# Performance work log

Hardware: AMD Instinct MI355X
Metric: run time of the kernel (lower is better)

Reference implementation:

```python
import jax, jax.numpy as jnp
import numpy as np

B, N, C = 64, 512, 1280


def setup_inputs() -> dict:
    key = jax.random.key(0)
    ks = jax.random.split(key, 10)
    scale = 0.02
    x = jax.random.normal(ks[0], (B, N, C), dtype=jnp.float32)
    Mask = jax.random.randint(ks[1], (B, N, N), 0, 2, dtype=jnp.int32)
    Wq = jax.random.normal(ks[2], (C, C), dtype=jnp.float32) * scale
    bq = jnp.zeros((C,), dtype=jnp.float32)
    Wk = jax.random.normal(ks[3], (C, C), dtype=jnp.float32) * scale
    bk = jnp.zeros((C,), dtype=jnp.float32)
    Wv = jax.random.normal(ks[4], (C, C), dtype=jnp.float32) * scale
    bv = jnp.zeros((C,), dtype=jnp.float32)
    Wr = jax.random.normal(ks[5], (C, C), dtype=jnp.float32) * scale
    br = jnp.zeros((C,), dtype=jnp.float32)
    return {"x": x, "Mask": Mask, "Wq": Wq, "bq": bq, "Wk": Wk, "bk": bk,
            "Wv": Wv, "bv": bv, "Wr": Wr, "br": br}


def reference(x, Mask, Wq, bq, Wk, bk, Wv, bv, Wr, br):
    # q, k, v: [B, N, C]
    q = x @ Wq + bq
    k = x @ Wk + bk
    v = x @ Wv + bv
    # scores[b, n, m] = q[b, n] . k[b, m]  -> [B, N, N]
    scores = jnp.einsum('bnc,bmc->bnm', q, k)
    # masked_fill BEFORE the scale divide, as in the original module
    scores = jnp.where(Mask == 0, jnp.float32(-1e20), scores)
    attn = jax.nn.softmax(scores / jnp.sqrt(jnp.float32(C)), axis=-1)
    # original: (V^T @ attn).permute -> out[b, n, c] = sum_m v[b, m, c] * attn[b, m, n]
    att_feat = jnp.einsum('bmc,bmn->bnc', v, attn)
    return att_feat @ Wr + br
```

## Files before the change

### kernel.cpp

```cpp
#include <hip/hip_runtime.h>
#include <hip/hip_bf16.h>

#define DI __device__ __forceinline__

typedef __attribute__((ext_vector_type(8))) short short8;
typedef __attribute__((ext_vector_type(4))) float f32x4;

DI unsigned short f2bf(float f) {
    union { float f; unsigned int u; } v; v.f = f;
    unsigned int r = v.u + 0x7FFFu + ((v.u >> 16) & 1u);
    return (unsigned short)(r >> 16);
}
DI float bf2f(unsigned short h) {
    union { unsigned int u; float f; } v; v.u = ((unsigned int)h) << 16;
    return v.f;
}

#define GLD16(g, l) __builtin_amdgcn_global_load_lds( \
    (const __attribute__((address_space(1))) void*)(g), \
    (__attribute__((address_space(3))) void*)(l), 16, 0, 0)

template<int EPI, int QKV>
__global__ __launch_bounds__(512, 2) void gemm256(
    const unsigned short* __restrict__ A, const unsigned short* __restrict__ Bt,
    void* __restrict__ Cout, const float* __restrict__ bias,
    const float* __restrict__ bias1, const float* __restrict__ bias2,
    const int* __restrict__ mask, int K, int lda, int ldb, int ldc,
    long sA, long sB, long sC, long sM, float scale)
{
    __shared__ unsigned short lds[65536];

    const unsigned gx = gridDim.x, gy = gridDim.y;
    unsigned lin = blockIdx.x + gx * (blockIdx.y + gy * blockIdx.z);
    const unsigned nwg = gx * gy * gridDim.z;
    lin = (lin & 7u) * (nwg >> 3) + (lin >> 3);
    int tn = lin % gx;
    const int tm = (lin / gx) % gy;
    const int z = lin / (gx * gy);

    if (QKV) {
        const int g = tn / 5; tn -= g * 5;
        Bt += (size_t)g * sB;
        Cout = (void*)((unsigned short*)Cout + (size_t)g * sC);
        if (g == 1) bias = bias1; else if (g == 2) bias = bias2;
    }

    const unsigned short* Ab = A + (long)z * sA + (size_t)(tm * 256) * lda;
    const unsigned short* Bb = Bt + (QKV ? 0 : (long)z * sB) + (size_t)(tn * 256) * ldb;

    const int tid = threadIdx.x, wave = tid >> 6, l = tid & 63;
    const int wr = wave >> 2, wc = wave & 3;

    const int srow = wave * 32 + (l >> 2);
    const int schunk = ((l & 3) ^ ((l >> 3) & 3)) * 8;
    const unsigned short* agS = Ab + (size_t)srow * lda + schunk;
    const unsigned short* bgS = Bb + (size_t)srow * ldb + schunk;
    unsigned short* ldsA0 = &lds[wave * 1024];
    unsigned short* ldsB0 = &lds[8192 + wave * 1024];

    const int rl = l & 15;
    const int cl8 = ((l >> 4) ^ ((l >> 1) & 3)) * 8;
    const int aoff = (wr * 128 + rl) * 32 + cl8;
    const int boff = 8192 + (wc * 64 + rl) * 32 + cl8;

#define REGOFF(buf, h) (((buf) * 2 + (h)) * 16384)
#define SA(t, h, buf) { const unsigned short* g_ = agS + (size_t)((t) * 64 + (h) * 32); \
    GLD16(g_, ldsA0 + REGOFF(buf, h)); \
    GLD16(g_ + (size_t)16 * lda, ldsA0 + REGOFF(buf, h) + 512); }
#define SB(t, h, buf) { const unsigned short* g_ = bgS + (size_t)((t) * 64 + (h) * 32); \
    GLD16(g_, ldsB0 + REGOFF(buf, h)); \
    GLD16(g_ + (size_t)16 * ldb, ldsB0 + REGOFF(buf, h) + 512); }

    f32x4 acc[8][4] = {};
    short8 bfr[4];

#define PHASE(mg, h, buf, RDB, STG, VMW) { \
    short8 af[4]; \
    if (RDB) { \
        _Pragma("unroll") for (int n = 0; n < 4; ++n) \
            bfr[n] = *(const short8*)&lds[REGOFF(buf, h) + boff + n * 512]; \
    } \
    _Pragma("unroll") for (int i = 0; i < 4; ++i) \
        af[i] = *(const short8*)&lds[REGOFF(buf, h) + aoff + ((mg) * 4 + i) * 512]; \
    STG; \
    __builtin_amdgcn_s_barrier(); \
    asm volatile("s_waitcnt lgkmcnt(0)" ::: "memory"); \
    __builtin_amdgcn_sched_barrier(0); \
    __builtin_amdgcn_s_setprio(1); \
    _Pragma("unroll") for (int i = 0; i < 4; ++i) \
        _Pragma("unroll") for (int n = 0; n < 4; ++n) \
            acc[(mg) * 4 + i][n] = __builtin_amdgcn_mfma_f32_16x16x32_bf16( \
                af[i], bfr[n], acc[(mg) * 4 + i][n], 0, 0, 0); \
    __builtin_amdgcn_s_setprio(0); \
    asm volatile("s_waitcnt " VMW ::: "memory"); \
    __builtin_amdgcn_s_barrier(); \
  }

    SA(0, 0, 0); SB(0, 0, 0); SA(0, 1, 0); SB(0, 1, 0); SA(1, 0, 1); SB(1, 0, 1);
    asm volatile("s_waitcnt vmcnt(8)" ::: "memory");
    __builtin_amdgcn_s_barrier();

    const int NI = K >> 7;
    for (int j = 0; j < NI - 1; ++j) {
        const int t = 2 * j;
        PHASE(0, 0, 0, 1, SA(t + 1, 1, 1), "vmcnt(8)")
        PHASE(1, 0, 0, 0, SB(t + 1, 1, 1), "vmcnt(8)")
        PHASE(0, 1, 0, 1, SA(t + 2, 0, 0), "vmcnt(8)")
        PHASE(1, 1, 0, 0, SB(t + 2, 0, 0), "vmcnt(8)")
        PHASE(0, 0, 1, 1, SA(t + 2, 1, 0), "vmcnt(8)")
        PHASE(1, 0, 1, 0, SB(t + 2, 1, 0), "vmcnt(8)")
        PHASE(0, 1, 1, 1, SA(t + 3, 0, 1), "vmcnt(8)")
        PHASE(1, 1, 1, 0, SB(t + 3, 0, 1), "vmcnt(8)")
    }
    {
        const int t = 2 * (NI - 1);
        PHASE(0, 0, 0, 1, SA(t + 1, 1, 1), "vmcnt(8)")
        PHASE(1, 0, 0, 0, SB(t + 1, 1, 1), "vmcnt(8)")
        PHASE(0, 1, 0, 1, ((void)0),       "vmcnt(8)")
        PHASE(1, 1, 0, 0, ((void)0),       "vmcnt(4)")
        PHASE(0, 0, 1, 1, ((void)0),       "vmcnt(4)")
        PHASE(1, 0, 1, 0, ((void)0),       "vmcnt(0)")
        PHASE(0, 1, 1, 1, ((void)0),       "vmcnt(0)")
        PHASE(1, 1, 1, 0, ((void)0),       "vmcnt(0)")
    }
#undef PHASE
#undef SA
#undef SB
#undef REGOFF

    const long cb = QKV ? 0 : (long)z * sC;
    const int row0 = tm * 256 + wr * 128 + (l >> 4) * 4;
    const int col0 = tn * 256 + wc * 64 + rl;
    #pragma unroll
    for (int mi = 0; mi < 8; ++mi) {
        #pragma unroll
        for (int n = 0; n < 4; ++n) {
            #pragma unroll
            for (int r = 0; r < 4; ++r) {
                const int row = row0 + mi * 16 + r;
                const int col = col0 + n * 16;
                float v = acc[mi][n][r];
                if (EPI == 0 || EPI == 3) v += bias[col];
                if (EPI == 1) {
                    v *= scale;
                    if (mask[(long)z * sM + (long)row * ldc + col] == 0)
                        v = -1e20f * scale;
                }
                if (EPI == 3)
                    ((float*)Cout)[cb + (long)row * ldc + col] = v;
                else
                    ((unsigned short*)Cout)[cb + (long)row * ldc + col] = f2bf(v);
            }
        }
    }
}

__global__ void transpose_w(const float* __restrict__ Wq, const float* __restrict__ Wk,
                            const float* __restrict__ Wv, const float* __restrict__ Wr,
                            unsigned short* __restrict__ Wt)
{
    const float* W = blockIdx.z == 0 ? Wq : blockIdx.z == 1 ? Wk : blockIdx.z == 2 ? Wv : Wr;
    unsigned short* dst = Wt + (size_t)blockIdx.z * 1280 * 1280;
    __shared__ float T[64][65];
    const int j0 = blockIdx.x * 64, k0 = blockIdx.y * 64;
    const int tid = threadIdx.x;
    for (int it = 0; it < 16; ++it) {
        int idx = it * 256 + tid;
        int r = idx >> 6, c = idx & 63;
        T[r][c] = W[(size_t)(k0 + r) * 1280 + j0 + c];
    }
    __syncthreads();
    for (int it = 0; it < 16; ++it) {
        int idx = it * 256 + tid;
        int r = idx >> 6, c = idx & 63;
        dst[(size_t)(j0 + r) * 1280 + k0 + c] = f2bf(T[c][r]);
    }
}

__global__ void cast_x(const float* __restrict__ x, unsigned short* __restrict__ xb, long n)
{
    long i = ((long)blockIdx.x * 256 + threadIdx.x) * 8;
    if (i + 8 > n) return;
    const float4* p = (const float4*)(x + i);
    float4 a = p[0], b = p[1];
    unsigned short o[8] = { f2bf(a.x), f2bf(a.y), f2bf(a.z), f2bf(a.w),
                            f2bf(b.x), f2bf(b.y), f2bf(b.z), f2bf(b.w) };
    *(short8*)(xb + i) = *(short8*)o;
}

#define SMS 514
__global__ void softmax_t(const unsigned short* __restrict__ S, unsigned short* __restrict__ Pt)
{
    __shared__ unsigned short T[64 * SMS];
    __shared__ float rmax[64], rinv[64];
    const int b = blockIdx.y, mb = blockIdx.x * 64;
    const int tid = threadIdx.x, lane = tid & 63, wave = tid >> 6;
    const unsigned short* src = S + ((size_t)b * 512 + mb) * 512;

    for (int rr = 0; rr < 16; ++rr) {
        int r = rr * 4 + wave;
        const unsigned int* s = (const unsigned int*)(src + (size_t)r * 512);
        unsigned int* t = (unsigned int*)&T[r * SMS];
        #pragma unroll
        for (int j = 0; j < 4; ++j) t[lane + j * 64] = s[lane + j * 64];
    }
    __syncthreads();

    {
        int r = tid >> 2, q = tid & 3;
        const unsigned short* row = &T[r * SMS + q * 128];
        float mx = -3.0e38f;
        for (int i = 0; i < 128; ++i) mx = fmaxf(mx, bf2f(row[i]));
        mx = fmaxf(mx, __shfl_xor(mx, 1));
        mx = fmaxf(mx, __shfl_xor(mx, 2));
        float s = 0.f;
        for (int i = 0; i < 128; ++i) s += expf(bf2f(row[i]) - mx);
        s += __shfl_xor(s, 1);
        s += __shfl_xor(s, 2);
        if (q == 0) { rmax[r] = mx; rinv[r] = 1.0f / s; }
    }
    __syncthreads();

    {
        int m = tid & 63, nq = tid >> 6;
        float mxm = rmax[m], rim = rinv[m];
        unsigned short* dst = Pt + (size_t)b * 512 * 512 + mb + m;
        for (int it = 0; it < 128; ++it) {
            int n = it * 4 + nq;
            float v = expf(bf2f(T[m * SMS + n]) - mxm) * rim;
            dst[(size_t)n * 512] = f2bf(v);
        }
    }
}

__global__ void transpose_v(const unsigned short* __restrict__ V, unsigned short* __restrict__ Vt)
{
    __shared__ unsigned short T[64][65];
    const int b = blockIdx.z;
    const int c0 = blockIdx.x * 64, m0 = blockIdx.y * 64;
    const int tid = threadIdx.x;
    const unsigned short* src = V + ((size_t)b * 512 + m0) * 1280 + c0;
    for (int it = 0; it < 16; ++it) {
        int idx = it * 256 + tid;
        int r = idx >> 6, c = idx & 63;
        T[r][c] = src[(size_t)r * 1280 + c];
    }
    __syncthreads();
    unsigned short* dst = Vt + ((size_t)b * 1280 + c0) * 512 + m0;
    for (int it = 0; it < 16; ++it) {
        int idx = it * 256 + tid;
        int r = idx >> 6, c = idx & 63;
        dst[(size_t)r * 512 + c] = T[c][r];
    }
}

extern "C" void kernel_launch(void* const* d_in, const int* in_sizes, int n_in,
                              void* d_out, int out_size, void* d_ws, size_t ws_size,
                              hipStream_t stream)
{
    const float* x   = (const float*)d_in[0];
    const int*  Mask = (const int*)d_in[1];
    const float* Wq  = (const float*)d_in[2];
    const float* bq  = (const float*)d_in[3];
    const float* Wk  = (const float*)d_in[4];
    const float* bk  = (const float*)d_in[5];
    const float* Wv  = (const float*)d_in[6];
    const float* bv  = (const float*)d_in[7];
    const float* Wr  = (const float*)d_in[8];
    const float* br  = (const float*)d_in[9];

    constexpr int N = 512, C = 1280;
    constexpr long MN = 32768;

    char* ws = (char*)d_ws;
    unsigned short* xb = (unsigned short*)ws;
    unsigned short* Wt = (unsigned short*)(ws + 83886080);
    unsigned short* Q  = (unsigned short*)(ws + 83886080 + 13107200);
    unsigned short* Km = Q + 41943040;
    unsigned short* V  = Km + 41943040;
    unsigned short* Sp = V + 41943040;
    unsigned short* Pt = Sp + 16777216;
    unsigned short* Vt = Q;
    unsigned short* att = xb;

    const float scale = 0.02795084971874737f;

    transpose_w<<<dim3(20, 20, 4), 256, 0, stream>>>(Wq, Wk, Wv, Wr, Wt);
    cast_x<<<dim3(20480), 256, 0, stream>>>(x, xb, MN * C);

    gemm256<0, 1><<<dim3(15, 128, 1), 512, 0, stream>>>(xb, Wt, (void*)Q, bq, bk, bv,
        nullptr, C, C, C, C, 0, 1638400L, 41943040L, 0, 0.f);

    gemm256<1, 0><<<dim3(2, 2, 64), 512, 0, stream>>>(Q, Km, (void*)Sp, nullptr, nullptr, nullptr,
        Mask, C, C, C, N, (long)N * C, (long)N * C, (long)N * N, (long)N * N, scale);

    softmax_t<<<dim3(8, 64), 256, 0, stream>>>(Sp, Pt);

    transpose_v<<<dim3(20, 8, 64), 256, 0, stream>>>(V, Vt);

    gemm256<2, 0><<<dim3(5, 2, 64), 512, 0, stream>>>(Pt, Vt, (void*)att, nullptr, nullptr, nullptr,
        nullptr, N, N, N, C, (long)N * N, (long)C * N, (long)N * C, 0, 0.f);

    gemm256<3, 0><<<dim3(5, 128, 1), 512, 0, stream>>>(att, Wt + 3 * 1638400, d_out, br, nullptr, nullptr,
        nullptr, C, C, C, C, 0, 0, 0, 0, 0.f);
}
```

Before: 722.5 us.

## Double-buffer LDS fragment registers to overlap reads with MFMA in GEMM

Restructures the GEMM main loop so the A/B fragments for the next phase are read from LDS into a second register set while the MFMAs for the current phase run, with one barrier per phase placed after the compute. The vmcnt waits are retuned to match the new staging order, and a final compute-only phase is added. Epilogue stores become nontemporal to reduce cache pollution. Doubling the fragment registers raises register pressure under launch_bounds(512,2), which could cause spills.

```diff
diff --git a/kernel.cpp b/kernel.cpp
--- a/kernel.cpp
+++ b/kernel.cpp
@@ -72,58 +72,72 @@
     GLD16(g_ + (size_t)16 * ldb, ldsB0 + REGOFF(buf, h) + 512); }
 
     f32x4 acc[8][4] = {};
-    short8 bfr[4];
-
-#define PHASE(mg, h, buf, RDB, STG, VMW) { \
-    short8 af[4]; \
-    if (RDB) { \
+    short8 af0[4], af1[4], bf0[4], bf1[4];
+
+#define PHASE(MGC, CUR, NXT, MGN, HN, BUFN, STG, VMW) { \
+    if (MGN == 0) { \
         _Pragma("unroll") for (int n = 0; n < 4; ++n) \
-            bfr[n] = *(const short8*)&lds[REGOFF(buf, h) + boff + n * 512]; \
+            bf##NXT[n] = *(const short8*)&lds[REGOFF(BUFN, HN) + boff + n * 512]; \
+    } else { \
+        _Pragma("unroll") for (int n = 0; n < 4; ++n) bf##NXT[n] = bf##CUR[n]; \
     } \
     _Pragma("unroll") for (int i = 0; i < 4; ++i) \
-        af[i] = *(const short8*)&lds[REGOFF(buf, h) + aoff + ((mg) * 4 + i) * 512]; \
+        af##NXT[i] = *(const short8*)&lds[REGOFF(BUFN, HN) + aoff + ((MGN) * 4 + i) * 512]; \
     STG; \
-    __builtin_amdgcn_s_barrier(); \
-    asm volatile("s_waitcnt lgkmcnt(0)" ::: "memory"); \
     __builtin_amdgcn_sched_barrier(0); \
     __builtin_amdgcn_s_setprio(1); \
     _Pragma("unroll") for (int i = 0; i < 4; ++i) \
         _Pragma("unroll") for (int n = 0; n < 4; ++n) \
-            acc[(mg) * 4 + i][n] = __builtin_amdgcn_mfma_f32_16x16x32_bf16( \
-                af[i], bfr[n], acc[(mg) * 4 + i][n], 0, 0, 0); \
+            acc[(MGC) * 4 + i][n] = __builtin_amdgcn_mfma_f32_16x16x32_bf16( \
+                af##CUR[i], bf##CUR[n], acc[(MGC) * 4 + i][n], 0, 0, 0); \
     __builtin_amdgcn_s_setprio(0); \
     asm volatile("s_waitcnt " VMW ::: "memory"); \
+    asm volatile("s_waitcnt lgkmcnt(0)" ::: "memory"); \
+    __builtin_amdgcn_sched_barrier(0); \
     __builtin_amdgcn_s_barrier(); \
+  }
+#define PHASELAST(MGC, CUR) { \
+    __builtin_amdgcn_s_setprio(1); \
+    _Pragma("unroll") for (int i = 0; i < 4; ++i) \
+        _Pragma("unroll") for (int n = 0; n < 4; ++n) \
+            acc[(MGC) * 4 + i][n] = __builtin_amdgcn_mfma_f32_16x16x32_bf16( \
+                af##CUR[i], bf##CUR[n], acc[(MGC) * 4 + i][n], 0, 0, 0); \
+    __builtin_amdgcn_s_setprio(0); \
   }
 
     SA(0, 0, 0); SB(0, 0, 0); SA(0, 1, 0); SB(0, 1, 0); SA(1, 0, 1); SB(1, 0, 1);
     asm volatile("s_waitcnt vmcnt(8)" ::: "memory");
     __builtin_amdgcn_s_barrier();
+    #pragma unroll
+    for (int n = 0; n < 4; ++n) bf0[n] = *(const short8*)&lds[REGOFF(0, 0) + boff + n * 512];
+    #pragma unroll
+    for (int i = 0; i < 4; ++i) af0[i] = *(const short8*)&lds[REGOFF(0, 0) + aoff + i * 512];
 
     const int NI = K >> 7;
     for (int j = 0; j < NI - 1; ++j) {
         const int t = 2 * j;
-        PHASE(0, 0, 0, 1, SA(t + 1, 1, 1), "vmcnt(8)")
-        PHASE(1, 0, 0, 0, SB(t + 1, 1, 1), "vmcnt(8)")
-        PHASE(0, 1, 0, 1, SA(t + 2, 0, 0), "vmcnt(8)")
-        PHASE(1, 1, 0, 0, SB(t + 2, 0, 0), "vmcnt(8)")
-        PHASE(0, 0, 1, 1, SA(t + 2, 1, 0), "vmcnt(8)")
-        PHASE(1, 0, 1, 0, SB(t + 2, 1, 0), "vmcnt(8)")
-        PHASE(0, 1, 1, 1, SA(t + 3, 0, 1), "vmcnt(8)")
-        PHASE(1, 1, 1, 0, SB(t + 3, 0, 1), "vmcnt(8)")
+        PHASE(0, 0, 1, 1, 0, 0, SA(t + 1, 1, 1), "vmcnt(6)")
+        PHASE(1, 1, 0, 0, 1, 0, SB(t + 1, 1, 1), "vmcnt(6)")
+        PHASE(0, 0, 1, 1, 1, 0, SA(t + 2, 0, 0), "vmcnt(6)")
+        PHASE(1, 1, 0, 0, 0, 1, SB(t + 2, 0, 0), "vmcnt(6)")
+        PHASE(0, 0, 1, 1, 0, 1, SA(t + 2, 1, 0), "vmcnt(6)")
+        PHASE(1, 1, 0, 0, 1, 1, SB(t + 2, 1, 0), "vmcnt(6)")
+        PHASE(0, 0, 1, 1, 1, 1, SA(t + 3, 0, 1), "vmcnt(6)")
+        PHASE(1, 1, 0, 0, 0, 0, SB(t + 3, 0, 1), "vmcnt(6)")
     }
     {
         const int t = 2 * (NI - 1);
-        PHASE(0, 0, 0, 1, SA(t + 1, 1, 1), "vmcnt(8)")
-        PHASE(1, 0, 0, 0, SB(t + 1, 1, 1), "vmcnt(8)")
-        PHASE(0, 1, 0, 1, ((void)0),       "vmcnt(8)")
-        PHASE(1, 1, 0, 0, ((void)0),       "vmcnt(4)")
-        PHASE(0, 0, 1, 1, ((void)0),       "vmcnt(4)")
-        PHASE(1, 0, 1, 0, ((void)0),       "vmcnt(0)")
-        PHASE(0, 1, 1, 1, ((void)0),       "vmcnt(0)")
-        PHASE(1, 1, 1, 0, ((void)0),       "vmcnt(0)")
+        PHASE(0, 0, 1, 1, 0, 0, SA(t + 1, 1, 1), "vmcnt(6)")
+        PHASE(1, 1, 0, 0, 1, 0, SB(t + 1, 1, 1), "vmcnt(6)")
+        PHASE(0, 0, 1, 1, 1, 0, ((void)0),       "vmcnt(4)")
+        PHASE(1, 1, 0, 0, 0, 1, ((void)0),       "vmcnt(2)")
+        PHASE(0, 0, 1, 1, 0, 1, ((void)0),       "vmcnt(0)")
+        PHASE(1, 1, 0, 0, 1, 1, ((void)0),       "vmcnt(0)")
+        PHASE(0, 0, 1, 1, 1, 1, ((void)0),       "vmcnt(0)")
+        PHASELAST(1, 1)
     }
 #undef PHASE
+#undef PHASELAST
 #undef SA
 #undef SB
 #undef REGOFF
@@ -147,9 +161,9 @@
                         v = -1e20f * scale;
                 }
                 if (EPI == 3)
-                    ((float*)Cout)[cb + (long)row * ldc + col] = v;
+                    __builtin_nontemporal_store(v, &((float*)Cout)[cb + (long)row * ldc + col]);
                 else
-                    ((unsigned short*)Cout)[cb + (long)row * ldc + col] = f2bf(v);
+                    __builtin_nontemporal_store(f2bf(v), &((unsigned short*)Cout)[cb + (long)row * ldc + col]);
             }
         }
     }
```

After: 820.2 us. 1.14x slower.

## Merge GEMM phases into four per iteration with split LDS waits

Applied to the files above, without the earlier changes.

Cuts the eight half-tile phases per K iteration to four. Each phase now loads all eight A fragments and the four B fragments, issues both the A and B global-to-LDS stage loads, and runs 32 MFMAs. The barrier before compute is dropped and a partial lgkmcnt(4) wait lets the first 16 MFMAs start while the last A fragment reads are still in flight. This halves the barrier and waitcnt count per tile. In exchange it holds more fragment registers, and removing the pre-compute barrier depends on the remaining barriers and the vmcnt waits being enough to keep the double-buffered LDS safe.

```diff
diff --git a/kernel.cpp b/kernel.cpp
--- a/kernel.cpp
+++ b/kernel.cpp
@@ -72,25 +72,29 @@
     GLD16(g_ + (size_t)16 * ldb, ldsB0 + REGOFF(buf, h) + 512); }
 
     f32x4 acc[8][4] = {};
-    short8 bfr[4];
-
-#define PHASE(mg, h, buf, RDB, STG, VMW) { \
-    short8 af[4]; \
-    if (RDB) { \
-        _Pragma("unroll") for (int n = 0; n < 4; ++n) \
-            bfr[n] = *(const short8*)&lds[REGOFF(buf, h) + boff + n * 512]; \
-    } \
+
+#define PHASE(buf, h, STG, VMW) { \
+    short8 af[8], bfv[4]; \
     _Pragma("unroll") for (int i = 0; i < 4; ++i) \
-        af[i] = *(const short8*)&lds[REGOFF(buf, h) + aoff + ((mg) * 4 + i) * 512]; \
+        af[i] = *(const short8*)&lds[REGOFF(buf, h) + aoff + i * 512]; \
+    _Pragma("unroll") for (int n = 0; n < 4; ++n) \
+        bfv[n] = *(const short8*)&lds[REGOFF(buf, h) + boff + n * 512]; \
+    _Pragma("unroll") for (int i = 4; i < 8; ++i) \
+        af[i] = *(const short8*)&lds[REGOFF(buf, h) + aoff + i * 512]; \
     STG; \
-    __builtin_amdgcn_s_barrier(); \
-    asm volatile("s_waitcnt lgkmcnt(0)" ::: "memory"); \
+    asm volatile("s_waitcnt lgkmcnt(4)" ::: "memory"); \
     __builtin_amdgcn_sched_barrier(0); \
     __builtin_amdgcn_s_setprio(1); \
     _Pragma("unroll") for (int i = 0; i < 4; ++i) \
         _Pragma("unroll") for (int n = 0; n < 4; ++n) \
-            acc[(mg) * 4 + i][n] = __builtin_amdgcn_mfma_f32_16x16x32_bf16( \
-                af[i], bfr[n], acc[(mg) * 4 + i][n], 0, 0, 0); \
+            acc[i][n] = __builtin_amdgcn_mfma_f32_16x16x32_bf16( \
+                af[i], bfv[n], acc[i][n], 0, 0, 0); \
+    asm volatile("s_waitcnt lgkmcnt(0)" ::: "memory"); \
+    __builtin_amdgcn_sched_barrier(0); \
+    _Pragma("unroll") for (int i = 4; i < 8; ++i) \
+        _Pragma("unroll") for (int n = 0; n < 4; ++n) \
+            acc[i][n] = __builtin_amdgcn_mfma_f32_16x16x32_bf16( \
+                af[i], bfv[n], acc[i][n], 0, 0, 0); \
     __builtin_amdgcn_s_setprio(0); \
     asm volatile("s_waitcnt " VMW ::: "memory"); \
     __builtin_amdgcn_s_barrier(); \
@@ -103,25 +107,17 @@
     const int NI = K >> 7;
     for (int j = 0; j < NI - 1; ++j) {
         const int t = 2 * j;
-        PHASE(0, 0, 0, 1, SA(t + 1, 1, 1), "vmcnt(8)")
-        PHASE(1, 0, 0, 0, SB(t + 1, 1, 1), "vmcnt(8)")
-        PHASE(0, 1, 0, 1, SA(t + 2, 0, 0), "vmcnt(8)")
-        PHASE(1, 1, 0, 0, SB(t + 2, 0, 0), "vmcnt(8)")
-        PHASE(0, 0, 1, 1, SA(t + 2, 1, 0), "vmcnt(8)")
-        PHASE(1, 0, 1, 0, SB(t + 2, 1, 0), "vmcnt(8)")
-        PHASE(0, 1, 1, 1, SA(t + 3, 0, 1), "vmcnt(8)")
-        PHASE(1, 1, 1, 0, SB(t + 3, 0, 1), "vmcnt(8)")
+        PHASE(0, 0, SA(t + 1, 1, 1) SB(t + 1, 1, 1), "vmcnt(8)")
+        PHASE(0, 1, SA(t + 2, 0, 0) SB(t + 2, 0, 0), "vmcnt(8)")
+        PHASE(1, 0, SA(t + 2, 1, 0) SB(t + 2, 1, 0), "vmcnt(8)")
+        PHASE(1, 1, SA(t + 3, 0, 1) SB(t + 3, 0, 1), "vmcnt(8)")
     }
     {
         const int t = 2 * (NI - 1);
-        PHASE(0, 0, 0, 1, SA(t + 1, 1, 1), "vmcnt(8)")
-        PHASE(1, 0, 0, 0, SB(t + 1, 1, 1), "vmcnt(8)")
-        PHASE(0, 1, 0, 1, ((void)0),       "vmcnt(8)")
-        PHASE(1, 1, 0, 0, ((void)0),       "vmcnt(4)")
-        PHASE(0, 0, 1, 1, ((void)0),       "vmcnt(4)")
-        PHASE(1, 0, 1, 0, ((void)0),       "vmcnt(0)")
-        PHASE(0, 1, 1, 1, ((void)0),       "vmcnt(0)")
-        PHASE(1, 1, 1, 0, ((void)0),       "vmcnt(0)")
+        PHASE(0, 0, SA(t + 1, 1, 1) SB(t + 1, 1, 1), "vmcnt(8)")
+        PHASE(0, 1, ((void)0),                       "vmcnt(4)")
+        PHASE(1, 0, ((void)0),                       "vmcnt(0)")
+        PHASE(1, 1, ((void)0),                       "vmcnt(0)")
     }
 #undef PHASE
 #undef SA
```

Result: no change. 732.1 us (+1.3%).
